# Optimization experiments

Hardware: AMD Instinct MI355X
Metric: run time of the kernel (lower is better)

The kernel has to match this reference:

```python
import jax, jax.numpy as jnp
import numpy as np

B, S, D, DQKV = 4, 2048, 1024, 1024

def setup_inputs() -> dict:
    key = jax.random.key(0)
    kx, kq, kk, kv = jax.random.split(key, 4)
    scale = 1.0 / np.sqrt(D)
    return {
        "x": jax.random.normal(kx, (B, S, D), dtype=jnp.float32),
        "wq": jax.random.normal(kq, (D, DQKV), dtype=jnp.float32) * scale,
        "wk": jax.random.normal(kk, (D, DQKV), dtype=jnp.float32) * scale,
        "wv": jax.random.normal(kv, (D, DQKV), dtype=jnp.float32) * scale,
    }

def reference(x, wq, wk, wv):
    # QKV projections: [B,S,D] @ [D,Dqkv] -> [B,S,Dqkv]
    q = jnp.einsum('bsd,de->bse', x, wq)
    k = jnp.einsum('bsd,de->bse', x, wk)
    v = jnp.einsum('bsd,de->bse', x, wv)
    # scores: [B,S,S], scaled by sqrt(dim_qkv)
    scores = jnp.einsum('bik,bjk->bij', q, k) / jnp.sqrt(jnp.asarray(DQKV, dtype=x.dtype))
    attn = jax.nn.softmax(scores, axis=-1)
    # output: [B,S,Dqkv]
    return jnp.einsum('bij,bjd->bid', attn, v)
```

## Files before the change

### kernel.cpp

```cpp
#include <hip/hip_runtime.h>
#include <cstdint>
#include <cstddef>

typedef __bf16 bf16;
typedef __bf16 bf16x4 __attribute__((ext_vector_type(4)));
typedef __bf16 bf16x8 __attribute__((ext_vector_type(8)));
typedef float  f32x4  __attribute__((ext_vector_type(4)));
typedef float  f32x16 __attribute__((ext_vector_type(16)));

#define BATCH 4
#define SEQ   2048
#define DIM   1024
#define LDP   2112

__device__ __forceinline__ bf16 to_bf16(float f) {
    unsigned u = __builtin_bit_cast(unsigned, f);
    u += 0x7fffu + ((u >> 16) & 1u);
    unsigned short h = (unsigned short)(u >> 16);
    return __builtin_bit_cast(bf16, h);
}

__device__ __forceinline__ void load16_lds(const bf16* g, bf16* l) {
    __builtin_amdgcn_global_load_lds(
        (__attribute__((address_space(1))) void*)(g),
        (__attribute__((address_space(3))) void*)(l),
        16, 0, 0);
}

#define BARRIER() do { asm volatile("" ::: "memory"); \
                       __builtin_amdgcn_s_barrier();  \
                       asm volatile("" ::: "memory"); } while (0)
#define LGKM0()   asm volatile("s_waitcnt lgkmcnt(0)" ::: "memory")
#define VM0()     asm volatile("s_waitcnt vmcnt(0)" ::: "memory")


__device__ __forceinline__ void stage_half(
    const bf16* __restrict__ srcRow0, int ld, int k0, bf16* dstHalfBase)
{
    const int tid  = threadIdx.x;
    const int wave = tid >> 6;
    const int lane = tid & 63;
    const int rg   = lane >> 3;
    const int scoff = ((lane & 7) ^ rg) * 8;
#pragma unroll
    for (int j = 0; j < 2; ++j) {
        const int r = wave * 16 + j * 8;
        load16_lds(srcRow0 + (size_t)(r + rg) * ld + k0 + scoff,
                   dstHalfBase + r * 64);
    }
}

__device__ __forceinline__ void gemm_big_core(
    const bf16* __restrict__ Ablk, const bf16* __restrict__ Bblk,
    int K, int lda, int ldb, bf16* As, bf16* Bs, f32x4 acc[8][4])
{
    const int tid  = threadIdx.x;
    const int lane = tid & 63;
    const int wave = tid >> 6;
    const int wr   = wave >> 2;
    const int wc   = wave & 3;
    const int r16  = lane & 15;
    const int g    = lane >> 4;
    const int r7   = r16 & 7;
    const int pk0  = ((g) ^ r7) * 8;
    const int pk1  = ((4 + g) ^ r7) * 8;
    const int arow = (wr * 128 + r16) * 64;
    const int brow = (wc * 64 + r16) * 64;
    const int NT   = K >> 6;

    stage_half(Bblk, ldb, 0, Bs);
    stage_half(Bblk + (size_t)128 * ldb, ldb, 0, Bs + 8192);
    stage_half(Ablk, lda, 0, As);
    stage_half(Ablk + (size_t)128 * lda, lda, 0, As + 8192);
    VM0();
    BARRIER();

#pragma unroll 2
    for (int t = 0; t < NT; ++t) {
        bf16* Ac = As + (t & 1) * 16384;
        bf16* Bc = Bs + (t & 1) * 16384;
        bf16* An = As + ((t + 1) & 1) * 16384;
        bf16* Bn = Bs + ((t + 1) & 1) * 16384;
        const int k1 = (t + 1) << 6;

        bf16x8 b[4][2], a[4][2], a2[4][2];
#pragma unroll
        for (int n = 0; n < 4; ++n) {
            b[n][0] = *(const bf16x8*)(Bc + brow + n * 1024 + pk0);
            b[n][1] = *(const bf16x8*)(Bc + brow + n * 1024 + pk1);
        }
#pragma unroll
        for (int m = 0; m < 4; ++m) {
            a[m][0] = *(const bf16x8*)(Ac + arow + m * 1024 + pk0);
            a[m][1] = *(const bf16x8*)(Ac + arow + m * 1024 + pk1);
        }
        if (t + 1 < NT) {
            stage_half(Bblk, ldb, k1, Bn);
            stage_half(Bblk + (size_t)128 * ldb, ldb, k1, Bn + 8192);
            stage_half(Ablk, lda, k1, An);
            stage_half(Ablk + (size_t)128 * lda, lda, k1, An + 8192);
        }
#pragma unroll
        for (int m = 0; m < 4; ++m)
#pragma unroll
            for (int n = 0; n < 4; ++n)
#pragma unroll
                for (int ks = 0; ks < 2; ++ks)
                    acc[m][n] = __builtin_amdgcn_mfma_f32_16x16x32_bf16(
                        a[m][ks], b[n][ks], acc[m][n], 0, 0, 0);
#pragma unroll
        for (int m = 0; m < 4; ++m) {
            a2[m][0] = *(const bf16x8*)(Ac + arow + 4096 + m * 1024 + pk0);
            a2[m][1] = *(const bf16x8*)(Ac + arow + 4096 + m * 1024 + pk1);
        }
#pragma unroll
        for (int m = 0; m < 4; ++m)
#pragma unroll
            for (int n = 0; n < 4; ++n)
#pragma unroll
                for (int ks = 0; ks < 2; ++ks)
                    acc[4 + m][n] = __builtin_amdgcn_mfma_f32_16x16x32_bf16(
                        a2[m][ks], b[n][ks], acc[4 + m][n], 0, 0, 0);

        LGKM0();
        if (t + 1 < NT) VM0();
        BARRIER();
    }
}

__device__ __forceinline__ void write_c256(
    bf16* __restrict__ Cb, int ldc, const f32x4 acc[8][4])
{
    const int lane = threadIdx.x & 63;
    const int wave = threadIdx.x >> 6;
    const int wr = wave >> 2, wc = wave & 3;
    const int r16 = lane & 15, g = lane >> 4;
    const int row0 = wr * 128 + g * 4;
    const int col0 = wc * 64 + r16;
#pragma unroll
    for (int m = 0; m < 8; ++m)
#pragma unroll
        for (int n = 0; n < 4; ++n)
#pragma unroll
            for (int rr = 0; rr < 4; ++rr)
                Cb[(size_t)(row0 + m * 16 + rr) * ldc + col0 + n * 16] =
                    to_bf16(acc[m][n][rr]);
}

__device__ __forceinline__ void stage_tiles(
    const bf16* __restrict__ Abase, const bf16* __restrict__ Bbase,
    int k0, int lda, int ldb, bf16* As, bf16* Bs)
{
    const int tid   = threadIdx.x;
    const int wave  = tid >> 6;
    const int lane  = tid & 63;
    const int srow0 = wave * 8 + (lane >> 3);
    const int scoff = (((lane & 7) ^ ((lane >> 3) & 7)) * 8);
    const int ldsW  = wave * 512;
#pragma unroll
    for (int j = 0; j < 4; ++j) {
        load16_lds(Abase + (size_t)(j * 32 + srow0) * lda + k0 + scoff,
                   As + j * 2048 + ldsW);
        load16_lds(Bbase + (size_t)(j * 32 + srow0) * ldb + k0 + scoff,
                   Bs + j * 2048 + ldsW);
    }
}

__device__ __forceinline__ void gemm_core64_32(
    const bf16* __restrict__ Abase, const bf16* __restrict__ Bbase,
    int K, int lda, int ldb, bf16* As, bf16* Bs, f32x16 acc[2][2])
{
    const int tid  = threadIdx.x;
    const int lane = tid & 63;
    const int wave = tid >> 6;
    const int wm   = (wave >> 1) * 64;
    const int wn   = (wave & 1) * 64;
    const int r32  = lane & 31;
    const int hi   = lane >> 5;

    for (int k0 = 0; k0 < K; k0 += 64) {
        __syncthreads();
        stage_tiles(Abase, Bbase, k0, lda, ldb, As, Bs);
        __syncthreads();
#pragma unroll
        for (int t = 0; t < 4; ++t) {
            bf16x8 af[2], bfr[2];
            const int p = (2 * t + hi) ^ (r32 & 7);
#pragma unroll
            for (int i = 0; i < 2; ++i) {
                af[i]  = *(const bf16x8*)(As + (wm + i * 32 + r32) * 64 + p * 8);
                bfr[i] = *(const bf16x8*)(Bs + (wn + i * 32 + r32) * 64 + p * 8);
            }
#pragma unroll
            for (int mi = 0; mi < 2; ++mi)
#pragma unroll
                for (int ni = 0; ni < 2; ++ni)
                    acc[mi][ni] = __builtin_amdgcn_mfma_f32_32x32x16_bf16(
                        af[mi], bfr[ni], acc[mi][ni], 0, 0, 0);
        }
    }
}

__device__ __forceinline__ int c32_row(int reg, int hi) {
    return (reg & 3) + 8 * (reg >> 2) + 4 * hi;
}

__global__ __launch_bounds__(512, 2) void proj_qk(
    const bf16* __restrict__ xb, const bf16* __restrict__ Wt,
    bf16* __restrict__ Q, bf16* __restrict__ Kb)
{
    __shared__ bf16 As[32768];
    __shared__ bf16 Bs[32768];
    f32x4 acc[8][4] = {};

    const int r = blockIdx.x;
    const int my = r >> 3, j = r & 7;
    const bf16* Ab = xb + (size_t)my * 256 * DIM;
    const bf16* Bb = Wt + (size_t)((j >> 2) ? DIM * DIM : 0)
                        + (size_t)(j & 3) * 256 * DIM;
    bf16* dst = (j >> 2) ? Kb : Q;
    bf16* Cb = dst + (size_t)my * 256 * DIM + (size_t)(j & 3) * 256;

    gemm_big_core(Ab, Bb, DIM, DIM, DIM, As, Bs, acc);
    write_c256(Cb, DIM, acc);
}

__global__ __launch_bounds__(512, 2) void proj_v(
    const bf16* __restrict__ xb, const bf16* __restrict__ Wt,
    bf16* __restrict__ Vt)
{
    __shared__ bf16 As[32768];
    __shared__ bf16 Bs[32768];
    f32x4 acc[8][4] = {};

    const int u = blockIdx.x;
    const int bz = u >> 5, w = u & 31;
    const int vy = w >> 3, vx = w & 7;
    const bf16* Ab = Wt + (size_t)2 * DIM * DIM + (size_t)vy * 256 * DIM;
    const bf16* Bb = xb + (size_t)bz * SEQ * DIM + (size_t)vx * 256 * DIM;
    bf16* Cb = Vt + (size_t)bz * DIM * LDP + (size_t)vy * 256 * LDP
                  + (size_t)vx * 256;

    gemm_big_core(Ab, Bb, DIM, DIM, DIM, As, Bs, acc);
    write_c256(Cb, LDP, acc);
}

__global__ __launch_bounds__(512, 2) void gemm_scores8(
    const bf16* __restrict__ Qm, const bf16* __restrict__ Kb,
    bf16* __restrict__ P, float* __restrict__ lsum)
{
    __shared__ bf16 As[32768];
    __shared__ bf16 Bs[32768];
    f32x4 acc[8][4] = {};

    const int d = blockIdx.x;
    const int bx = d & 7, by = (d >> 3) & 7, bz = d >> 6;
    const bf16* Ab = Qm + (size_t)bz * SEQ * DIM + (size_t)by * 256 * DIM;
    const bf16* Bb = Kb + (size_t)bz * SEQ * DIM + (size_t)bx * 256 * DIM;
    gemm_big_core(Ab, Bb, DIM, DIM, DIM, As, Bs, acc);

    bf16* Cb  = P + (size_t)bz * SEQ * LDP;
    float* ls = lsum + (size_t)bz * SEQ;
    const int lane = threadIdx.x & 63;
    const int wave = threadIdx.x >> 6;
    const int wr = wave >> 2, wc = wave & 3;
    const int r16 = lane & 15, g = lane >> 4;
    const int rowB = by * 256 + wr * 128 + g * 4;
    const int colB = bx * 256 + wc * 64 + r16;
#pragma unroll
    for (int m = 0; m < 8; ++m)
#pragma unroll
        for (int rr = 0; rr < 4; ++rr) {
            float s = 0.0f;
#pragma unroll
            for (int n = 0; n < 4; ++n) {
                const float e = __expf(acc[m][n][rr] * 0.03125f);
                s += e;
                Cb[(size_t)(rowB + m * 16 + rr) * LDP + colB + n * 16] = to_bf16(e);
            }
            s += __shfl_xor(s, 1);
            s += __shfl_xor(s, 2);
            s += __shfl_xor(s, 4);
            s += __shfl_xor(s, 8);
            if (r16 == 0)
                atomicAdd(ls + rowB + m * 16 + rr, s);
        }
}

__global__ __launch_bounds__(256, 4) void gemm_pv(
    const bf16* __restrict__ P, const bf16* __restrict__ Vt, float* __restrict__ C,
    const float* __restrict__ lsum)
{
    __shared__ bf16 As[8192];
    __shared__ bf16 Bs[8192];
    f32x16 acc[2][2] = {};

    const int d = blockIdx.x + 8 * (blockIdx.y + 16 * blockIdx.z);
    const int c = d & 7, j = d >> 3;
    const int bx = j & 7;
    const int p = c + 8 * (j >> 3);
    const int by = p & 15, bz = p >> 4;

    const bf16* Ab = P  + (size_t)bz * SEQ * LDP + (size_t)by * 128 * LDP;
    const bf16* Bb = Vt + (size_t)bz * DIM * LDP + (size_t)bx * 128 * LDP;
    float* Cb = C + (size_t)bz * SEQ * DIM;
    gemm_core64_32(Ab, Bb, SEQ, LDP, LDP, As, Bs, acc);

    const int lane = threadIdx.x & 63;
    const int wave = threadIdx.x >> 6;
    const int hi = lane >> 5, r32 = lane & 31;
    const int wm = (wave >> 1) * 64, wn = (wave & 1) * 64;
    const int rowBase = by * 128 + wm;
    const int colBase = bx * 128 + wn + r32;
    const float* ls = lsum + (size_t)bz * SEQ;
#pragma unroll
    for (int mi = 0; mi < 2; ++mi)
#pragma unroll
        for (int reg = 0; reg < 16; ++reg) {
            const int row = rowBase + mi * 32 + c32_row(reg, hi);
            const float inv = __builtin_amdgcn_rcpf(ls[row]);
#pragma unroll
            for (int ni = 0; ni < 2; ++ni)
                Cb[(size_t)row * DIM + colBase + ni * 32] = acc[mi][ni][reg] * inv;
        }
}

__global__ __launch_bounds__(256) void prep(
    const float* __restrict__ x,  const float* __restrict__ wq,
    const float* __restrict__ wk, const float* __restrict__ wv,
    bf16* __restrict__ xb, bf16* __restrict__ Wt, float* __restrict__ lsum)
{
    __shared__ float tile[32][33];
    const int b = blockIdx.x;
    const int tid = threadIdx.x;
    if (b < 8192) {
        const size_t i = ((size_t)b * 256 + tid) * 4;
        const float4 v = *(const float4*)(x + i);
        bf16x4 o = { to_bf16(v.x), to_bf16(v.y), to_bf16(v.z), to_bf16(v.w) };
        *(bf16x4*)(xb + i) = o;
    } else if (b < 8192 + 3072) {
        const int t   = b - 8192;
        const int sel = t >> 10;
        const int n0  = (t & 31) * 32;
        const int k0  = ((t >> 5) & 31) * 32;
        const float* w = (sel == 0) ? wq : (sel == 1) ? wk : wv;
        const int tx = tid & 31, ty = tid >> 5;
#pragma unroll
        for (int j = 0; j < 32; j += 8)
            tile[ty + j][tx] = w[(size_t)(k0 + ty + j) * 1024 + n0 + tx];
        __syncthreads();
        bf16* dst = Wt + (size_t)sel * 1024 * 1024;
#pragma unroll
        for (int j = 0; j < 32; j += 8)
            dst[(size_t)(n0 + ty + j) * 1024 + k0 + tx] = to_bf16(tile[tx][ty + j]);
    } else {
#pragma unroll
        for (int i = 0; i < 32; ++i)
            lsum[i * 256 + tid] = 0.0f;
    }
}

extern "C" void kernel_launch(void* const* d_in, const int* in_sizes, int n_in,
                              void* d_out, int out_size, void* d_ws, size_t ws_size,
                              hipStream_t stream)
{
    const float* x  = (const float*)d_in[0];
    const float* wq = (const float*)d_in[1];
    const float* wk = (const float*)d_in[2];
    const float* wv = (const float*)d_in[3];
    float* out = (float*)d_out;
    char* ws = (char*)d_ws;

    bf16*  xb   = (bf16*)(ws);
    bf16*  Wt   = (bf16*)(ws + (16u << 20));
    bf16*  Q    = (bf16*)(ws + (22u << 20));
    bf16*  Kb   = (bf16*)(ws + (38u << 20));
    bf16*  Vt   = (bf16*)(ws + (54u << 20));
    bf16*  P    = (bf16*)(ws + (72u << 20));
    float* lsum = (float*)(ws + (108u << 20));

    prep<<<dim3(8192 + 3072 + 1), dim3(256), 0, stream>>>(
        x, wq, wk, wv, xb, Wt, lsum);

    proj_qk<<<dim3(256), dim3(512), 0, stream>>>(xb, Wt, Q, Kb);
    proj_v<<<dim3(128), dim3(512), 0, stream>>>(xb, Wt, Vt);

    gemm_scores8<<<dim3(256), dim3(512), 0, stream>>>(Q, Kb, P, lsum);

    gemm_pv<<<dim3(8, 16, 4), dim3(256), 0, stream>>>(P, Vt, out, lsum);
}
```

Measured before the change: 233.7 us.

## Use double-buffered 256x128 GEMM core for V projection and PV

Adds a 256x128 variant of the big double-buffered, prefetching GEMM core. proj_v now uses it so it launches 256 blocks instead of 128, filling more CUs. The PV GEMM is replaced: the old 128x128 single-buffered kernel with its full sync per k-step becomes a 512-thread 256x128 kernel that overlaps the next tile's loads with MFMA. The cost is larger LDS per block and fewer resident blocks, and PV drops from 512 blocks to 256.

```diff
diff --git a/kernel.cpp b/kernel.cpp
--- a/kernel.cpp
+++ b/kernel.cpp
@@ -6,7 +6,6 @@
 typedef __bf16 bf16x4 __attribute__((ext_vector_type(4)));
 typedef __bf16 bf16x8 __attribute__((ext_vector_type(8)));
 typedef float  f32x4  __attribute__((ext_vector_type(4)));
-typedef float  f32x16 __attribute__((ext_vector_type(16)));
 
 #define BATCH 4
 #define SEQ   2048
@@ -128,6 +127,69 @@
     }
 }
 
+__device__ __forceinline__ void gemm_big_core_n128(
+    const bf16* __restrict__ Ablk, const bf16* __restrict__ Bblk,
+    int K, int lda, int ldb, bf16* As, bf16* Bs, f32x4 acc[4][4])
+{
+    const int tid  = threadIdx.x;
+    const int lane = tid & 63;
+    const int wave = tid >> 6;
+    const int wr   = wave >> 1;
+    const int wc   = wave & 1;
+    const int r16  = lane & 15;
+    const int g    = lane >> 4;
+    const int r7   = r16 & 7;
+    const int pk0  = ((g) ^ r7) * 8;
+    const int pk1  = ((4 + g) ^ r7) * 8;
+    const int arow = (wr * 64 + r16) * 64;
+    const int brow = (wc * 64 + r16) * 64;
+    const int NT   = K >> 6;
+
+    stage_half(Ablk, lda, 0, As);
+    stage_half(Ablk + (size_t)128 * lda, lda, 0, As + 8192);
+    stage_half(Bblk, ldb, 0, Bs);
+    VM0();
+    BARRIER();
+
+#pragma unroll 2
+    for (int t = 0; t < NT; ++t) {
+        bf16* Ac = As + (t & 1) * 16384;
+        bf16* Bc = Bs + (t & 1) * 8192;
+        bf16* An = As + ((t + 1) & 1) * 16384;
+        bf16* Bn = Bs + ((t + 1) & 1) * 8192;
+        const int k1 = (t + 1) << 6;
+
+        bf16x8 a[4][2], b[4][2];
+#pragma unroll
+        for (int n = 0; n < 4; ++n) {
+            b[n][0] = *(const bf16x8*)(Bc + brow + n * 1024 + pk0);
+            b[n][1] = *(const bf16x8*)(Bc + brow + n * 1024 + pk1);
+        }
+#pragma unroll
+        for (int m = 0; m < 4; ++m) {
+            a[m][0] = *(const bf16x8*)(Ac + arow + m * 1024 + pk0);
+            a[m][1] = *(const bf16x8*)(Ac + arow + m * 1024 + pk1);
+        }
+        if (t + 1 < NT) {
+            stage_half(Ablk, lda, k1, An);
+            stage_half(Ablk + (size_t)128 * lda, lda, k1, An + 8192);
+            stage_half(Bblk, ldb, k1, Bn);
+        }
+#pragma unroll
+        for (int m = 0; m < 4; ++m)
+#pragma unroll
+            for (int n = 0; n < 4; ++n)
+#pragma unroll
+                for (int ks = 0; ks < 2; ++ks)
+                    acc[m][n] = __builtin_amdgcn_mfma_f32_16x16x32_bf16(
+                        a[m][ks], b[n][ks], acc[m][n], 0, 0, 0);
+
+        LGKM0();
+        if (t + 1 < NT) VM0();
+        BARRIER();
+    }
+}
+
 __device__ __forceinline__ void write_c256(
     bf16* __restrict__ Cb, int ldc, const f32x4 acc[8][4])
 {
@@ -147,62 +209,23 @@
                     to_bf16(acc[m][n][rr]);
 }
 
-__device__ __forceinline__ void stage_tiles(
-    const bf16* __restrict__ Abase, const bf16* __restrict__ Bbase,
-    int k0, int lda, int ldb, bf16* As, bf16* Bs)
-{
-    const int tid   = threadIdx.x;
-    const int wave  = tid >> 6;
-    const int lane  = tid & 63;
-    const int srow0 = wave * 8 + (lane >> 3);
-    const int scoff = (((lane & 7) ^ ((lane >> 3) & 7)) * 8);
-    const int ldsW  = wave * 512;
-#pragma unroll
-    for (int j = 0; j < 4; ++j) {
-        load16_lds(Abase + (size_t)(j * 32 + srow0) * lda + k0 + scoff,
-                   As + j * 2048 + ldsW);
-        load16_lds(Bbase + (size_t)(j * 32 + srow0) * ldb + k0 + scoff,
-                   Bs + j * 2048 + ldsW);
-    }
-}
-
-__device__ __forceinline__ void gemm_core64_32(
-    const bf16* __restrict__ Abase, const bf16* __restrict__ Bbase,
-    int K, int lda, int ldb, bf16* As, bf16* Bs, f32x16 acc[2][2])
-{
-    const int tid  = threadIdx.x;
-    const int lane = tid & 63;
-    const int wave = tid >> 6;
-    const int wm   = (wave >> 1) * 64;
-    const int wn   = (wave & 1) * 64;
-    const int r32  = lane & 31;
-    const int hi   = lane >> 5;
-
-    for (int k0 = 0; k0 < K; k0 += 64) {
-        __syncthreads();
-        stage_tiles(Abase, Bbase, k0, lda, ldb, As, Bs);
-        __syncthreads();
-#pragma unroll
-        for (int t = 0; t < 4; ++t) {
-            bf16x8 af[2], bfr[2];
-            const int p = (2 * t + hi) ^ (r32 & 7);
-#pragma unroll
-            for (int i = 0; i < 2; ++i) {
-                af[i]  = *(const bf16x8*)(As + (wm + i * 32 + r32) * 64 + p * 8);
-                bfr[i] = *(const bf16x8*)(Bs + (wn + i * 32 + r32) * 64 + p * 8);
-            }
-#pragma unroll
-            for (int mi = 0; mi < 2; ++mi)
-#pragma unroll
-                for (int ni = 0; ni < 2; ++ni)
-                    acc[mi][ni] = __builtin_amdgcn_mfma_f32_32x32x16_bf16(
-                        af[mi], bfr[ni], acc[mi][ni], 0, 0, 0);
-        }
-    }
-}
-
-__device__ __forceinline__ int c32_row(int reg, int hi) {
-    return (reg & 3) + 8 * (reg >> 2) + 4 * hi;
+__device__ __forceinline__ void write_c128n(
+    bf16* __restrict__ Cb, int ldc, const f32x4 acc[4][4])
+{
+    const int lane = threadIdx.x & 63;
+    const int wave = threadIdx.x >> 6;
+    const int wr = wave >> 1, wc = wave & 1;
+    const int r16 = lane & 15, g = lane >> 4;
+    const int row0 = wr * 64 + g * 4;
+    const int col0 = wc * 64 + r16;
+#pragma unroll
+    for (int m = 0; m < 4; ++m)
+#pragma unroll
+        for (int n = 0; n < 4; ++n)
+#pragma unroll
+            for (int rr = 0; rr < 4; ++rr)
+                Cb[(size_t)(row0 + m * 16 + rr) * ldc + col0 + n * 16] =
+                    to_bf16(acc[m][n][rr]);
 }
 
 __global__ __launch_bounds__(512, 2) void proj_qk(
@@ -230,19 +253,18 @@
     bf16* __restrict__ Vt)
 {
     __shared__ bf16 As[32768];
-    __shared__ bf16 Bs[32768];
-    f32x4 acc[8][4] = {};
-
-    const int u = blockIdx.x;
-    const int bz = u >> 5, w = u & 31;
-    const int vy = w >> 3, vx = w & 7;
+    __shared__ bf16 Bs[16384];
+    f32x4 acc[4][4] = {};
+
+    const int d = blockIdx.x;
+    const int vx = d & 15, vy = (d >> 4) & 3, bz = d >> 6;
     const bf16* Ab = Wt + (size_t)2 * DIM * DIM + (size_t)vy * 256 * DIM;
-    const bf16* Bb = xb + (size_t)bz * SEQ * DIM + (size_t)vx * 256 * DIM;
+    const bf16* Bb = xb + (size_t)bz * SEQ * DIM + (size_t)vx * 128 * DIM;
     bf16* Cb = Vt + (size_t)bz * DIM * LDP + (size_t)vy * 256 * LDP
-                  + (size_t)vx * 256;
-
-    gemm_big_core(Ab, Bb, DIM, DIM, DIM, As, Bs, acc);
-    write_c256(Cb, LDP, acc);
+                  + (size_t)vx * 128;
+
+    gemm_big_core_n128(Ab, Bb, DIM, DIM, DIM, As, Bs, acc);
+    write_c128n(Cb, LDP, acc);
 }
 
 __global__ __launch_bounds__(512, 2) void gemm_scores8(
@@ -287,41 +309,37 @@
         }
 }
 
-__global__ __launch_bounds__(256, 4) void gemm_pv(
-    const bf16* __restrict__ P, const bf16* __restrict__ Vt, float* __restrict__ C,
-    const float* __restrict__ lsum)
-{
-    __shared__ bf16 As[8192];
-    __shared__ bf16 Bs[8192];
-    f32x16 acc[2][2] = {};
-
-    const int d = blockIdx.x + 8 * (blockIdx.y + 16 * blockIdx.z);
-    const int c = d & 7, j = d >> 3;
-    const int bx = j & 7;
-    const int p = c + 8 * (j >> 3);
-    const int by = p & 15, bz = p >> 4;
-
-    const bf16* Ab = P  + (size_t)bz * SEQ * LDP + (size_t)by * 128 * LDP;
+__global__ __launch_bounds__(512, 2) void gemm_pv8(
+    const bf16* __restrict__ P, const bf16* __restrict__ Vt,
+    float* __restrict__ C, const float* __restrict__ lsum)
+{
+    __shared__ bf16 As[32768];
+    __shared__ bf16 Bs[16384];
+    f32x4 acc[4][4] = {};
+
+    const int d = blockIdx.x;
+    const int bx = d & 7, by = (d >> 3) & 7, bz = d >> 6;
+    const bf16* Ab = P  + (size_t)bz * SEQ * LDP + (size_t)by * 256 * LDP;
     const bf16* Bb = Vt + (size_t)bz * DIM * LDP + (size_t)bx * 128 * LDP;
+    gemm_big_core_n128(Ab, Bb, SEQ, LDP, LDP, As, Bs, acc);
+
     float* Cb = C + (size_t)bz * SEQ * DIM;
-    gemm_core64_32(Ab, Bb, SEQ, LDP, LDP, As, Bs, acc);
-
+    const float* ls = lsum + (size_t)bz * SEQ;
     const int lane = threadIdx.x & 63;
     const int wave = threadIdx.x >> 6;
-    const int hi = lane >> 5, r32 = lane & 31;
-    const int wm = (wave >> 1) * 64, wn = (wave & 1) * 64;
-    const int rowBase = by * 128 + wm;
-    const int colBase = bx * 128 + wn + r32;
-    const float* ls = lsum + (size_t)bz * SEQ;
-#pragma unroll
-    for (int mi = 0; mi < 2; ++mi)
-#pragma unroll
-        for (int reg = 0; reg < 16; ++reg) {
-            const int row = rowBase + mi * 32 + c32_row(reg, hi);
+    const int wr = wave >> 1, wc = wave & 1;
+    const int r16 = lane & 15, g = lane >> 4;
+    const int row0 = by * 256 + wr * 64 + g * 4;
+    const int col0 = bx * 128 + wc * 64 + r16;
+#pragma unroll
+    for (int m = 0; m < 4; ++m)
+#pragma unroll
+        for (int rr = 0; rr < 4; ++rr) {
+            const int row = row0 + m * 16 + rr;
             const float inv = __builtin_amdgcn_rcpf(ls[row]);
 #pragma unroll
-            for (int ni = 0; ni < 2; ++ni)
-                Cb[(size_t)row * DIM + colBase + ni * 32] = acc[mi][ni][reg] * inv;
+            for (int n = 0; n < 4; ++n)
+                Cb[(size_t)row * DIM + col0 + n * 16] = acc[m][n][rr] * inv;
         }
 }
 
@@ -383,9 +401,9 @@
         x, wq, wk, wv, xb, Wt, lsum);
 
     proj_qk<<<dim3(256), dim3(512), 0, stream>>>(xb, Wt, Q, Kb);
-    proj_v<<<dim3(128), dim3(512), 0, stream>>>(xb, Wt, Vt);
+    proj_v<<<dim3(256), dim3(512), 0, stream>>>(xb, Wt, Vt);
 
     gemm_scores8<<<dim3(256), dim3(512), 0, stream>>>(Q, Kb, P, lsum);
 
-    gemm_pv<<<dim3(8, 16, 4), dim3(256), 0, stream>>>(P, Vt, out, lsum);
-}
+    gemm_pv8<<<dim3(256), dim3(512), 0, stream>>>(P, Vt, out, lsum);
+}
```

After: 236.6 us. No clear change (+1.3%).
